# Kernel tuning notes

Hardware: AMD Instinct MI355X
Metric: run time of the kernel (lower is better)

Reference implementation:

```python
import math
import jax, jax.numpy as jnp
import numpy as np

# ---- static configuration (matches init_kwargs) ----
B_IN, B_OUT = 32, 16
F_IN, F_OUT = 16, 32
BATCH = 8
N_GRID = 72
SCALING = 1.0 / math.sqrt(N_GRID * F_IN * (B_OUT ** 3) / (B_IN ** 3))

_LOGFACT = np.concatenate([[0.0], np.cumsum(np.log(np.arange(1, 200, dtype=np.float64)))])


def _spectral_indices(b):
    """Flattened (l, m, n) index lists for all degrees l < b. nspec = sum (2l+1)^2."""
    ls, ms, ns = [], [], []
    for l in range(b):
        for m in range(-l, l + 1):
            for n in range(-l, l + 1):
                ls.append(l); ms.append(m); ns.append(n)
    return np.array(ls), np.array(ms), np.array(ns)

_LS, _MS, _NS = _spectral_indices(B_OUT)
_BETA_IN = (np.pi * (2 * np.arange(2 * B_IN) + 1) / (4 * B_IN)).astype(np.float32)
_BETA_OUT = (np.pi * (2 * np.arange(2 * B_OUT) + 1) / (4 * B_OUT)).astype(np.float32)


def _wigner_d_table(b, beta):
    """Small Wigner-d matrices d^l_{mn}(beta) for all l < b, stacked per flattened
    (l,m,n) spectral index -> [nspec, len(beta)]. Coefficients are numpy constants;
    beta may be a traced jnp array (explicit Wigner formula, exponents masked)."""
    beta = jnp.asarray(beta, jnp.float32)
    c = jnp.cos(beta / 2.0)
    s = jnp.sin(beta / 2.0)
    blocks = []
    for l in range(b):
        r = np.arange(-l, l + 1)
        M = r[:, None, None]; N = r[None, :, None]
        K = np.arange(0, 2 * l + 1)[None, None, :]
        valid = (l + M - K >= 0) & (l - N - K >= 0) & (N - M + K >= 0)
        Kc = np.where(valid, K, 0)
        lg = 0.5 * (_LOGFACT[l + M] + _LOGFACT[l - M] + _LOGFACT[l + N] + _LOGFACT[l - N])
        lg = lg - (_LOGFACT[Kc]
                   + _LOGFACT[np.where(valid, l + M - K, 0)]
                   + _LOGFACT[np.where(valid, l - N - K, 0)]
                   + _LOGFACT[np.where(valid, N - M + K, 0)])
        coef = np.where(valid, (-1.0) ** Kc * np.exp(lg), 0.0).astype(np.float32)
        e1 = np.where(valid, 2 * l + M - N - 2 * K, 0)  # exponent of cos(beta/2)
        e2 = np.where(valid, N - M + 2 * K, 0)          # exponent of sin(beta/2)
        term = (c[None, None, None, :] ** e1[..., None]) * (s[None, None, None, :] ** e2[..., None])
        d_l = jnp.einsum('mnk,mnkj->mnj', jnp.asarray(coef), term)
        blocks.append(d_l.reshape((2 * l + 1) ** 2, -1))
    return jnp.concatenate(blocks, axis=0)


def _quadrature_weights(b):
    """Driscoll-Healy quadrature weights over beta; also folds in the 1/(2b)^2
    normalization of the unnormalized alpha/gamma FFT."""
    j = np.arange(2 * b)
    k = np.arange(b)
    inner = (np.sin((2 * j[:, None] + 1) * (2 * k[None, :] + 1) * np.pi / (4 * b)) / (2 * k + 1)).sum(1)
    w = (2.0 / b) * np.sin(np.pi * (2 * j + 1) / (4 * b)) * inner
    return (w / (2 * b) ** 2).astype(np.float32)


def setup_inputs() -> dict:
    key = jax.random.key(0)
    k1, k2, k3 = jax.random.split(key, 3)
    x = jax.random.normal(k1, (BATCH, F_IN, 2 * B_IN, 2 * B_IN, 2 * B_IN), jnp.float32)
    kernel = jax.random.uniform(k2, (F_IN, F_OUT, N_GRID), jnp.float32, -0.05, 0.05)
    bias = jnp.zeros((F_OUT,), jnp.float32)
    g = jax.random.uniform(k3, (N_GRID, 3), jnp.float32)
    grid_euler = g * jnp.asarray([2 * np.pi, np.pi, 2 * np.pi], jnp.float32)  # (alpha, beta, gamma)
    return {"x": x, "kernel": kernel, "bias": bias, "grid_euler": grid_euler}


def reference(x, kernel, bias, grid_euler):
    mi_in = jnp.asarray(_MS % (2 * B_IN)); ni_in = jnp.asarray(_NS % (2 * B_IN))
    mi_out = jnp.asarray(_MS % (2 * B_OUT)); ni_out = jnp.asarray(_NS % (2 * B_OUT))

    # ---- so3_rfft(x, b_out): FFT over alpha/gamma + Wigner-d quadrature over beta ----
    Xf = jnp.fft.fftn(x.astype(jnp.complex64), axes=(2, 4))      # [B,Fi,2b(m),2b(beta),2b(n)]
    spec = Xf[:, :, mi_in, :, ni_in]                              # [nspec, B, Fi, 2b_in]
    Wan = _wigner_d_table(B_OUT, _BETA_IN) * jnp.asarray(_quadrature_weights(B_IN))[None, :]
    xc = jnp.einsum('sbfj,sj->sbf', spec, Wan.astype(jnp.complex64))  # [nspec, B, Fi]

    # ---- so3_rft(kernel*scaling, b_out, grid): direct Fourier transform of grid kernel ----
    alpha, beta_g, gamma = grid_euler[:, 0], grid_euler[:, 1], grid_euler[:, 2]
    dg = _wigner_d_table(B_OUT, beta_g)                           # [nspec, G]
    phase = jnp.exp(-1j * (jnp.asarray(_MS, jnp.float32)[:, None] * alpha[None, :]
                           + jnp.asarray(_NS, jnp.float32)[:, None] * gamma[None, :]))
    D = dg.astype(jnp.complex64) * phase.astype(jnp.complex64)
    yc = jnp.einsum('iog,sg->sio', (kernel * SCALING).astype(jnp.complex64), D)  # [nspec, Fi, Fo]

    # ---- per-degree block-diagonal matmul (SO(3) convolution theorem) ----
    zs = []
    off = 0
    for l in range(B_OUT):
        d = 2 * l + 1
        xb = xc[off:off + d * d].reshape(d, d, BATCH, F_IN)
        yb = yc[off:off + d * d].reshape(d, d, F_IN, F_OUT)
        zb = jnp.einsum('mkbi,knio->mnbo', xb, yb)                # (2l+1)x(2l+1) complex GEMM
        zs.append(zb.reshape(d * d, BATCH, F_OUT))
        off += d * d
    zc = jnp.concatenate(zs, axis=0)                              # [nspec, B, Fo]

    # ---- so3_rifft: Wigner-d synthesis over beta + inverse FFT over alpha/gamma ----
    Wsy = _wigner_d_table(B_OUT, _BETA_OUT) * jnp.asarray(2 * _LS + 1, jnp.float32)[:, None]
    contrib = jnp.einsum('sbf,sj->sjbf', zc, Wsy.astype(jnp.complex64))  # [nspec, 2b_out, B, Fo]
    n = 2 * B_OUT
    Xo = jnp.zeros((n, n, n, BATCH, F_OUT), jnp.complex64)
    Xo = Xo.at[mi_out, :, ni_out].add(contrib)                    # scatter per (m, n) frequency
    out = jnp.fft.ifftn(Xo, axes=(0, 2)).real * float(n * n)      # plain Fourier sum convention
    out = jnp.transpose(out, (3, 4, 0, 1, 2))                     # [B, Fo, 2b_out, 2b_out, 2b_out]
    return out + bias[None, :, None, None, None]
```

## Files before the change

kernel.cpp:

```cpp
#include <hip/hip_runtime.h>
#include <math.h>

#define PI_D 3.141592653589793238462643383279502884
#define PI_F 3.14159265358979323846f
#define SCALING_F (1.0f/12.0f)

__constant__ int c_OFF[17] = {0,1,10,35,84,165,286,455,680,969,1330,1771,2300,2925,3654,4495,5456};
__constant__ int c_Z8[17] = {0,1,4,9,16,34,56,82,112,163,220,283,352,452,560,676,800};

__device__ __forceinline__ void s_to_lmn(int s, int& l, int& m, int& n) {
    int ll = 15;
    while (s < c_OFF[ll]) --ll;
    int r = s - c_OFF[ll];
    int d = 2*ll + 1;
    l = ll;
    m = r / d - ll;
    n = r % d - ll;
}

__device__ __forceinline__ void build_tables_par(double beta, double* lf, double* cp, double* sp) {
    if (threadIdx.x < 64) {
        int i = threadIdx.x;
        lf[i] = lgamma((double)(i + 1));
        double cb = cos(beta*0.5), sb = sin(beta*0.5);
        cp[i] = (i == 0) ? 1.0 : exp((double)i * log(cb));
        sp[i] = (i == 0) ? 1.0 : exp((double)i * log(sb));
    }
}

__device__ double wigner_d_dev(int l, int m, int n,
                               const double* lf, const double* cp, const double* sp) {
    int kmin = m - n; if (kmin < 0) kmin = 0;
    int kmax = l + m; { int k2 = l - n; if (k2 < kmax) kmax = k2; }
    double pref = 0.5*(lf[l+m] + lf[l-m] + lf[l+n] + lf[l-n]);
    double acc = 0.0;
    for (int k = kmin; k <= kmax; ++k) {
        double lg = pref - (lf[k] + lf[l+m-k] + lf[l-n-k] + lf[n-m+k]);
        double t = exp(lg) * cp[2*l + m - n - 2*k] * sp[n - m + 2*k];
        acc += (k & 1) ? -t : t;
    }
    return acc;
}

__global__ void __launch_bounds__(256) k_wigner_in(float* WanT) {
    __shared__ double lf[64], cp[64], sp[64];
    __shared__ double tsum[32];
    __shared__ double wq;
    int j = blockIdx.x >> 2;
    int chunk = blockIdx.x & 3;
    double beta = PI_D * (2*j + 1) / 128.0;
    build_tables_par(beta, lf, cp, sp);
    if (threadIdx.x >= 64 && threadIdx.x < 96) {
        int k = threadIdx.x - 64;
        tsum[k] = sin((double)(2*j+1)*(2*k+1)*PI_D/128.0) / (double)(2*k+1);
    }
    __syncthreads();
    if (threadIdx.x == 0) {
        double inner = 0.0;
        for (int k = 0; k < 32; ++k) inner += tsum[k];
        wq = (2.0/32.0) * sin(PI_D*(2*j+1)/128.0) * inner / 4096.0;
    }
    __syncthreads();
    int s0 = chunk*1364, s1 = s0 + 1364; if (s1 > 5456) s1 = 5456;
    for (int s = s0 + threadIdx.x; s < s1; s += 256) {
        int l, m, n; s_to_lmn(s, l, m, n);
        WanT[j*5456 + s] = (float)(wigner_d_dev(l, m, n, lf, cp, sp) * wq);
    }
}

__global__ void __launch_bounds__(256) k_wigner_out(float* WsyT) {
    __shared__ double lf[64], cp[64], sp[64];
    int j = blockIdx.x >> 2;
    int chunk = blockIdx.x & 3;
    build_tables_par(PI_D*(2*j+1)/64.0, lf, cp, sp);
    __syncthreads();
    int s0 = chunk*1364, s1 = s0 + 1364; if (s1 > 5456) s1 = 5456;
    for (int s = s0 + threadIdx.x; s < s1; s += 256) {
        int l, m, n; s_to_lmn(s, l, m, n);
        WsyT[j*5456 + s] = (float)(wigner_d_dev(l, m, n, lf, cp, sp) * (double)(2*l+1));
    }
}

__global__ void __launch_bounds__(256) k_wigner_grid(const float* ge, float2* D) {
    __shared__ double lf[64], cp[64], sp[64];
    int g = blockIdx.x >> 2;
    int chunk = blockIdx.x & 3;
    double beta = (double)ge[g*3 + 1];
    double alp  = (double)ge[g*3 + 0];
    double gam  = (double)ge[g*3 + 2];
    build_tables_par(beta, lf, cp, sp);
    __syncthreads();
    int s0 = chunk*1364, s1 = s0 + 1364; if (s1 > 5456) s1 = 5456;
    for (int s = s0 + threadIdx.x; s < s1; s += 256) {
        int l, m, n; s_to_lmn(s, l, m, n);
        double dv = wigner_d_dev(l, m, n, lf, cp, sp);
        double th = m*alp + n*gam;
        double sn, cs; sincos(th, &sn, &cs);
        D[s*72 + g] = make_float2((float)(dv*cs), (float)(-dv*sn));
    }
}

__global__ void __launch_bounds__(256) k_yc(const float* kern, const float2* D, float2* yc) {
    __shared__ float2 Ds[4][72];
    int s0 = blockIdx.x * 4;
    for (int t = threadIdx.x; t < 288; t += 256) {
        int ss = t / 72, g = t - ss*72;
        Ds[ss][g] = D[(size_t)(s0 + ss)*72 + g];
    }
    __syncthreads();
    for (int io = threadIdx.x; io < 512; io += 256) {
        const float* kp = kern + io*72;
        float2 a0 = {0,0}, a1 = {0,0}, a2 = {0,0}, a3 = {0,0};
        for (int g = 0; g < 72; ++g) {
            float kv = kp[g];
            a0.x = fmaf(kv, Ds[0][g].x, a0.x); a0.y = fmaf(kv, Ds[0][g].y, a0.y);
            a1.x = fmaf(kv, Ds[1][g].x, a1.x); a1.y = fmaf(kv, Ds[1][g].y, a1.y);
            a2.x = fmaf(kv, Ds[2][g].x, a2.x); a2.y = fmaf(kv, Ds[2][g].y, a2.y);
            a3.x = fmaf(kv, Ds[3][g].x, a3.x); a3.y = fmaf(kv, Ds[3][g].y, a3.y);
        }
        yc[(size_t)(s0+0)*512 + io] = make_float2(a0.x*SCALING_F, a0.y*SCALING_F);
        yc[(size_t)(s0+1)*512 + io] = make_float2(a1.x*SCALING_F, a1.y*SCALING_F);
        yc[(size_t)(s0+2)*512 + io] = make_float2(a2.x*SCALING_F, a2.y*SCALING_F);
        yc[(size_t)(s0+3)*512 + io] = make_float2(a3.x*SCALING_F, a3.y*SCALING_F);
    }
}

__global__ void __launch_bounds__(256) k_fft(const float* x, float2* Fx) {
    __shared__ float  xs[64][66];
    __shared__ float2 T1s[16][66];
    __shared__ float2 tw2[16][66];
    int blk = blockIdx.x;
    int bf = blk >> 6, j = blk & 63;
    const float* xp = x + (size_t)bf*262144 + j*64;
    for (int t = threadIdx.x; t < 1024; t += 256) {
        int a = t >> 4, g4 = (t & 15) << 2;
        float4 v = *(const float4*)(xp + (size_t)a*4096 + g4);
        *(float2*)&xs[a][g4]     = make_float2(v.x, v.y);
        *(float2*)&xs[a][g4 + 2] = make_float2(v.z, v.w);
    }
    for (int t = threadIdx.x; t < 1024; t += 256) {
        int n = t >> 6, g = t & 63;
        float sn, cs;
        sincosf(-2.0f*PI_F*(float)((n*g) & 63)/64.0f, &sn, &cs);
        tw2[n][g] = make_float2(cs, sn);
    }
    __syncthreads();
    {
        int a  = threadIdx.x & 63;
        int n0 = (threadIdx.x >> 6) << 2;
        float2 c0 = {0,0}, c1 = {0,0}, c2 = {0,0}, c3 = {0,0};
        for (int g = 0; g < 64; g += 2) {
            float2 xv = *(const float2*)&xs[a][g];
            float4 w0 = *(const float4*)&tw2[n0    ][g];
            float4 w1 = *(const float4*)&tw2[n0 + 1][g];
            float4 w2 = *(const float4*)&tw2[n0 + 2][g];
            float4 w3 = *(const float4*)&tw2[n0 + 3][g];
            c0.x = fmaf(xv.x, w0.x, c0.x); c0.y = fmaf(xv.x, w0.y, c0.y);
            c0.x = fmaf(xv.y, w0.z, c0.x); c0.y = fmaf(xv.y, w0.w, c0.y);
            c1.x = fmaf(xv.x, w1.x, c1.x); c1.y = fmaf(xv.x, w1.y, c1.y);
            c1.x = fmaf(xv.y, w1.z, c1.x); c1.y = fmaf(xv.y, w1.w, c1.y);
            c2.x = fmaf(xv.x, w2.x, c2.x); c2.y = fmaf(xv.x, w2.y, c2.y);
            c2.x = fmaf(xv.y, w2.z, c2.x); c2.y = fmaf(xv.y, w2.w, c2.y);
            c3.x = fmaf(xv.x, w3.x, c3.x); c3.y = fmaf(xv.x, w3.y, c3.y);
            c3.x = fmaf(xv.y, w3.z, c3.x); c3.y = fmaf(xv.y, w3.w, c3.y);
        }
        T1s[n0    ][a] = c0;
        T1s[n0 + 1][a] = c1;
        T1s[n0 + 2][a] = c2;
        T1s[n0 + 3][a] = c3;
    }
    __syncthreads();
    {
        int nn = threadIdx.x & 15, mmg = threadIdx.x >> 4;
        int mm0 = mmg*2, mm1 = mm0 + 1;
        int am0 = mm0 >= 15 ? mm0 - 15 : 15 - mm0;
        int am1 = mm1 >= 15 ? mm1 - 15 : 15 - mm1;
        if (am1 > 15) am1 = 15;
        float sg0 = mm0 >= 15 ? 1.f : -1.f;
        float sg1 = mm1 >= 15 ? 1.f : -1.f;
        float2 c0 = {0,0}, c1 = {0,0};
        for (int a = 0; a < 64; a += 2) {
            float4 t01 = *(const float4*)&T1s[nn][a];
            float4 wa  = *(const float4*)&tw2[am0][a];
            float4 wb  = *(const float4*)&tw2[am1][a];
            float way0 = wa.y*sg0, way1 = wa.w*sg0;
            float wby0 = wb.y*sg1, wby1 = wb.w*sg1;
            c0.x += t01.x*wa.x - t01.y*way0;
            c0.y += t01.x*way0 + t01.y*wa.x;
            c0.x += t01.z*wa.z - t01.w*way1;
            c0.y += t01.z*way1 + t01.w*wa.z;
            c1.x += t01.x*wb.x - t01.y*wby0;
            c1.y += t01.x*wby0 + t01.y*wb.x;
            c1.x += t01.z*wb.z - t01.w*wby1;
            c1.y += t01.z*wby1 + t01.w*wb.z;
        }
        float2* outp = Fx + (size_t)blk*496;
        outp[mm0*16 + nn] = c0;
        if (mm1 < 31) outp[mm1*16 + nn] = c1;
    }
}

__global__ void __launch_bounds__(256) k_xc(const float2* Fx, const float* WanT, float2* xc) {
    __shared__ float2 Fsh[31][65];
    int blk = blockIdx.x;
    int bf = blk / 31, mm = blk - bf*31;
    int m = mm - 15;
    const float2* fp = Fx + (size_t)bf * 64 * 496;
    for (int t = threadIdx.x; t < 1024; t += 256) {
        int j = t >> 4, nn = t & 15;
        Fsh[nn + 15][j] = fp[j*496 + mm*16 + nn];
    }
    for (int t = threadIdx.x; t < 1024; t += 256) {
        int j = t >> 4, nn = t & 15;
        if (nn > 0) {
            float2 v = fp[j*496 + (30 - mm)*16 + nn];
            Fsh[15 - nn][j] = make_float2(v.x, -v.y);
        }
    }
    __syncthreads();
    int am = m < 0 ? -m : m;
    int q = threadIdx.x;
    int l = am;
    while (l <= 15 && q >= 2*l + 1) { q -= 2*l + 1; ++l; }
    if (l <= 15) {
        int n = q - l;
        int d = 2*l + 1;
        int s = c_OFF[l] + (m + l)*d + (n + l);
        const float* wp = WanT + s;
        const float2* frow = Fsh[n + 15];
        float ar = 0.f, ai = 0.f;
        for (int j2 = 0; j2 < 64; ++j2) {
            float w = wp[(size_t)j2*5456];
            ar = fmaf(w, frow[j2].x, ar);
            ai = fmaf(w, frow[j2].y, ai);
        }
        xc[(size_t)s*128 + bf] = make_float2(ar, ai);
    }
}

__global__ void __launch_bounds__(256) k_z(const float2* xc, const float2* yc, float2* zc) {
    __shared__ float2 Ash[2][16][66];
    __shared__ float2 Bsh[2][512];
    int blk = 799 - blockIdx.x;
    int l = 0;
    while (l < 15 && blk >= c_Z8[l+1]) ++l;
    int r = blk - c_Z8[l];
    int d = 2*l + 1;
    int mt = r / d;
    int n0 = r - mt*d;
    int m0 = mt*8;
    int off = c_OFF[l];

    int tx = threadIdx.x & 15, ty = threadIdx.x >> 4;
    int o0 = tx*2;

    int mloc_s = threadIdx.x >> 5;
    int bf0    = (threadIdx.x & 31) << 2;
    int bs     = bf0 >> 4;
    int i0s    = bf0 & 15;
    int mrow_s = m0 + mloc_s; if (mrow_s > d-1) mrow_s = d-1;
    const float2* xrow = xc + (size_t)(off + mrow_s*d)*128 + bf0;
    int io0 = threadIdx.x * 2;
    const float2* yrow = yc + (size_t)(off + n0)*512 + io0;

    float4 apf0, apf1, bpf;
    apf0 = *(const float4*)(xrow);
    apf1 = *(const float4*)(xrow + 2);
    bpf  = *(const float4*)(yrow);
    Ash[0][i0s+0][mloc_s*8+bs] = make_float2(apf0.x, apf0.y);
    Ash[0][i0s+1][mloc_s*8+bs] = make_float2(apf0.z, apf0.w);
    Ash[0][i0s+2][mloc_s*8+bs] = make_float2(apf1.x, apf1.y);
    Ash[0][i0s+3][mloc_s*8+bs] = make_float2(apf1.z, apf1.w);
    *(float4*)&Bsh[0][io0] = bpf;
    __syncthreads();

    float2 acc[4][2];
    #pragma unroll
    for (int jm = 0; jm < 4; ++jm) { acc[jm][0] = make_float2(0.f,0.f); acc[jm][1] = make_float2(0.f,0.f); }

    for (int k = 0; k < d; ++k) {
        int cur = k & 1;
        if (k + 1 < d) {
            const float2* xr = xrow + (size_t)(k+1)*128;
            const float2* yr = yrow + (size_t)(k+1)*d*512;
            apf0 = *(const float4*)(xr);
            apf1 = *(const float4*)(xr + 2);
            bpf  = *(const float4*)(yr);
        }
        #pragma unroll
        for (int i = 0; i < 16; ++i) {
            const float4* ap = (const float4*)&Ash[cur][i][ty*4];
            float4 a01 = ap[0], a23 = ap[1];
            float4 b01 = *(const float4*)&Bsh[cur][i*32 + o0];
            float2 av[4] = {{a01.x,a01.y},{a01.z,a01.w},{a23.x,a23.y},{a23.z,a23.w}};
            float2 bv[2] = {{b01.x,b01.y},{b01.z,b01.w}};
            #pragma unroll
            for (int jm = 0; jm < 4; ++jm) {
                acc[jm][0].x += av[jm].x*bv[0].x - av[jm].y*bv[0].y;
                acc[jm][0].y += av[jm].x*bv[0].y + av[jm].y*bv[0].x;
                acc[jm][1].x += av[jm].x*bv[1].x - av[jm].y*bv[1].y;
                acc[jm][1].y += av[jm].x*bv[1].y + av[jm].y*bv[1].x;
            }
        }
        if (k + 1 < d) {
            int nxt = cur ^ 1;
            Ash[nxt][i0s+0][mloc_s*8+bs] = make_float2(apf0.x, apf0.y);
            Ash[nxt][i0s+1][mloc_s*8+bs] = make_float2(apf0.z, apf0.w);
            Ash[nxt][i0s+2][mloc_s*8+bs] = make_float2(apf1.x, apf1.y);
            Ash[nxt][i0s+3][mloc_s*8+bs] = make_float2(apf1.z, apf1.w);
            *(float4*)&Bsh[nxt][io0] = bpf;
            __syncthreads();
        }
    }
    #pragma unroll
    for (int jm = 0; jm < 4; ++jm) {
        int mb = ty*4 + jm;
        int mrow = m0 + (mb >> 3);
        int b = mb & 7;
        if (mrow < d) {
            size_t base = (size_t)(off + mrow*d + n0)*256 + b*32 + o0;
            zc[base]     = acc[jm][0];
            zc[base + 1] = acc[jm][1];
        }
    }
}

__global__ void __launch_bounds__(256) k_su(const float2* zc, const float* WsyT, float2* U) {
    __shared__ float wsh[496];
    __shared__ float2 tw[32];
    int blk = blockIdx.x;
    int mmi = blk >> 5, j = blk & 31;
    int m = mmi - 15;
    int am = m < 0 ? -m : m;
    for (int t = threadIdx.x; t < 496; t += 256) {
        int l = t / 31, nn = t - l*31;
        int n = nn - 15, an = n < 0 ? -n : n;
        float w = 0.f;
        if (l >= am && l >= an) {
            int s = c_OFF[l] + (m + l)*(2*l + 1) + (n + l);
            w = WsyT[(size_t)j*5456 + s];
        }
        wsh[t] = w;
    }
    if (threadIdx.x < 32) {
        float sn, cs;
        sincosf(2.0f*PI_F*(float)threadIdx.x/32.0f, &sn, &cs);
        tw[threadIdx.x] = make_float2(cs, sn);
    }
    __syncthreads();
    float2 acc[32];
    #pragma unroll
    for (int g = 0; g < 32; ++g) acc[g] = make_float2(0.f, 0.f);
    for (int nni = 0; nni < 31; ++nni) {
        int n = nni - 15, an = n < 0 ? -n : n;
        int lmin = am > an ? am : an;
        float2 sv = make_float2(0.f, 0.f);
        for (int l = lmin; l < 16; ++l) {
            int s = c_OFF[l] + (m + l)*(2*l + 1) + (n + l);
            float2 zv = zc[(size_t)s*256 + threadIdx.x];
            float w = wsh[l*31 + nni];
            sv.x = fmaf(w, zv.x, sv.x);
            sv.y = fmaf(w, zv.y, sv.y);
        }
        int step = (nni + 17) & 31;
        int t = 0;
        #pragma unroll
        for (int g = 0; g < 32; ++g) {
            float2 w = tw[t];
            acc[g].x += sv.x*w.x - sv.y*w.y;
            acc[g].y += sv.x*w.y + sv.y*w.x;
            t = (t + step) & 31;
        }
    }
    float2* up = U + (((size_t)j*256 + threadIdx.x)*31 + mmi)*32;
    #pragma unroll
    for (int g = 0; g < 32; ++g) up[g] = acc[g];
}

__global__ void __launch_bounds__(256) k_out(const float2* U, const float* bias, float* out) {
    __shared__ float2 Ush[992];
    __shared__ float2 tw[32];
    int blk = blockIdx.x;
    int bo = blk >> 5, j = blk & 31;
    const float2* up = U + ((size_t)j*256 + bo)*992;
    for (int t = threadIdx.x; t < 992; t += 256) Ush[t] = up[t];
    if (threadIdx.x < 32) {
        float sn, cs;
        sincosf(2.0f*PI_F*(float)threadIdx.x/32.0f, &sn, &cs);
        tw[threadIdx.x] = make_float2(cs, sn);
    }
    __syncthreads();
    float bv = bias[bo & 31];
    int a  = threadIdx.x >> 3;
    int g0 = (threadIdx.x & 7) << 2;
    float ac0 = bv, ac1 = bv, ac2 = bv, ac3 = bv;
    for (int mmi = 0; mmi < 31; ++mmi) {
        int t = (((mmi + 17) & 31) * a) & 31;
        float2 w = tw[t];
        const float2* ur = Ush + mmi*32 + g0;
        float2 u0 = ur[0], u1 = ur[1], u2 = ur[2], u3 = ur[3];
        ac0 += u0.x*w.x - u0.y*w.y;
        ac1 += u1.x*w.x - u1.y*w.y;
        ac2 += u2.x*w.x - u2.y*w.y;
        ac3 += u3.x*w.x - u3.y*w.y;
    }
    float4 res = make_float4(ac0, ac1, ac2, ac3);
    *(float4*)(out + (((size_t)bo*32 + a)*32 + j)*32 + g0) = res;
}

extern "C" void kernel_launch(void* const* d_in, const int* in_sizes, int n_in,
                              void* d_out, int out_size, void* d_ws, size_t ws_size,
                              hipStream_t stream) {
    const float* x    = (const float*)d_in[0];
    const float* kern = (const float*)d_in[1];
    const float* bias = (const float*)d_in[2];
    const float* ge   = (const float*)d_in[3];
    float* out = (float*)d_out;
    char* ws = (char*)d_ws;

    float*  WsyT = (float*) (ws);
    float2* zc   = (float2*)(ws +    698368);
    float2* U    = (float2*)(ws +  11872256);
    float*  WanT = (float*) (ws +  11872256);
    float2* D    = (float2*)(ws +  13268992);
    float2* yc   = (float2*)(ws +  16411648);
    float2* Fx   = (float2*)(ws +  38759424);
    float2* xc   = (float2*)(ws +  71265280);

    k_wigner_in  <<< 256, 256, 0, stream>>>(WanT);
    k_wigner_out <<< 128, 256, 0, stream>>>(WsyT);
    k_wigner_grid<<< 288, 256, 0, stream>>>(ge, D);
    k_yc         <<<1364, 256, 0, stream>>>(kern, D, yc);
    k_fft        <<<8192, 256, 0, stream>>>(x, Fx);
    k_xc         <<<3968, 256, 0, stream>>>(Fx, WanT, xc);
    k_z          <<< 800, 256, 0, stream>>>(xc, yc, zc);
    k_su         <<< 992, 256, 0, stream>>>(zc, WsyT, U);
    k_out        <<<8192, 256, 0, stream>>>(U, bias, out);
}
```

Measured before the change: 635.2 us.

## Split the k_z reduction over k into chunks of 8 with atomic accumulation

The per-degree complex GEMM kernel now splits its reduction dimension k into chunks of 8, which raises the grid from 800 to 2720 blocks. The goal is to shorten the long serial k loops for high degrees and improve load balance across CUs. Partial sums are combined with float atomicAdd into zc whenever a degree has more than one m-tile, so zc is zeroed with a memset up front. The cost is extra atomic traffic, the memset, and a summation order that is no longer deterministic.

```diff
diff --git a/kernel.cpp b/kernel.cpp
--- a/kernel.cpp
+++ b/kernel.cpp
@@ -6,7 +6,7 @@
 #define SCALING_F (1.0f/12.0f)
 
 __constant__ int c_OFF[17] = {0,1,10,35,84,165,286,455,680,969,1330,1771,2300,2925,3654,4495,5456};
-__constant__ int c_Z8[17] = {0,1,4,9,16,34,56,82,112,163,220,283,352,452,560,676,800};
+__constant__ int c_ZB[17] = {0,1,4,9,16,52,96,148,208,361,532,721,928,1328,1760,2224,2720};
 
 __device__ __forceinline__ void s_to_lmn(int s, int& l, int& m, int& n) {
     int ll = 15;
@@ -241,15 +241,20 @@
 __global__ void __launch_bounds__(256) k_z(const float2* xc, const float2* yc, float2* zc) {
     __shared__ float2 Ash[2][16][66];
     __shared__ float2 Bsh[2][512];
-    int blk = 799 - blockIdx.x;
+    int blk = 2719 - blockIdx.x;
     int l = 0;
-    while (l < 15 && blk >= c_Z8[l+1]) ++l;
-    int r = blk - c_Z8[l];
+    while (l < 15 && blk >= c_ZB[l+1]) ++l;
+    int r = blk - c_ZB[l];
     int d = 2*l + 1;
-    int mt = r / d;
-    int n0 = r - mt*d;
+    int mtc = (d + 7) >> 3;
+    int mt = r % mtc;
+    int t2 = r / mtc;
+    int n0 = t2 % d;
+    int chunk = t2 / d;
     int m0 = mt*8;
     int off = c_OFF[l];
+    int k0 = chunk*8;
+    int k1 = k0 + 8; if (k1 > d) k1 = d;
 
     int tx = threadIdx.x & 15, ty = threadIdx.x >> 4;
     int o0 = tx*2;
@@ -264,9 +269,9 @@
     const float2* yrow = yc + (size_t)(off + n0)*512 + io0;
 
     float4 apf0, apf1, bpf;
-    apf0 = *(const float4*)(xrow);
-    apf1 = *(const float4*)(xrow + 2);
-    bpf  = *(const float4*)(yrow);
+    apf0 = *(const float4*)(xrow + (size_t)k0*128);
+    apf1 = *(const float4*)(xrow + (size_t)k0*128 + 2);
+    bpf  = *(const float4*)(yrow + (size_t)k0*d*512);
     Ash[0][i0s+0][mloc_s*8+bs] = make_float2(apf0.x, apf0.y);
     Ash[0][i0s+1][mloc_s*8+bs] = make_float2(apf0.z, apf0.w);
     Ash[0][i0s+2][mloc_s*8+bs] = make_float2(apf1.x, apf1.y);
@@ -278,9 +283,9 @@
     #pragma unroll
     for (int jm = 0; jm < 4; ++jm) { acc[jm][0] = make_float2(0.f,0.f); acc[jm][1] = make_float2(0.f,0.f); }
 
-    for (int k = 0; k < d; ++k) {
-        int cur = k & 1;
-        if (k + 1 < d) {
+    for (int k = k0; k < k1; ++k) {
+        int cur = (k - k0) & 1;
+        if (k + 1 < k1) {
             const float2* xr = xrow + (size_t)(k+1)*128;
             const float2* yr = yrow + (size_t)(k+1)*d*512;
             apf0 = *(const float4*)(xr);
@@ -302,7 +307,7 @@
                 acc[jm][1].y += av[jm].x*bv[1].y + av[jm].y*bv[1].x;
             }
         }
-        if (k + 1 < d) {
+        if (k + 1 < k1) {
             int nxt = cur ^ 1;
             Ash[nxt][i0s+0][mloc_s*8+bs] = make_float2(apf0.x, apf0.y);
             Ash[nxt][i0s+1][mloc_s*8+bs] = make_float2(apf0.z, apf0.w);
@@ -319,8 +324,16 @@
         int b = mb & 7;
         if (mrow < d) {
             size_t base = (size_t)(off + mrow*d + n0)*256 + b*32 + o0;
-            zc[base]     = acc[jm][0];
-            zc[base + 1] = acc[jm][1];
+            if (mtc == 1) {
+                zc[base]     = acc[jm][0];
+                zc[base + 1] = acc[jm][1];
+            } else {
+                float* zp = (float*)(zc + base);
+                atomicAdd(zp + 0, acc[jm][0].x);
+                atomicAdd(zp + 1, acc[jm][0].y);
+                atomicAdd(zp + 2, acc[jm][1].x);
+                atomicAdd(zp + 3, acc[jm][1].y);
+            }
         }
     }
 }
@@ -427,13 +440,15 @@
     float2* Fx   = (float2*)(ws +  38759424);
     float2* xc   = (float2*)(ws +  71265280);
 
+    hipMemsetAsync(zc, 0, 11173888, stream);
+
     k_wigner_in  <<< 256, 256, 0, stream>>>(WanT);
     k_wigner_out <<< 128, 256, 0, stream>>>(WsyT);
     k_wigner_grid<<< 288, 256, 0, stream>>>(ge, D);
     k_yc         <<<1364, 256, 0, stream>>>(kern, D, yc);
     k_fft        <<<8192, 256, 0, stream>>>(x, Fx);
     k_xc         <<<3968, 256, 0, stream>>>(Fx, WanT, xc);
-    k_z          <<< 800, 256, 0, stream>>>(xc, yc, zc);
+    k_z          <<<2720, 256, 0, stream>>>(xc, yc, zc);
     k_su         <<< 992, 256, 0, stream>>>(zc, WsyT, U);
     k_out        <<<8192, 256, 0, stream>>>(U, bias, out);
 }
```

After: 673.5 us. +6.0%, slower.
